# Optimization experiments

Measured on AMD Instinct MI355X. Metric: run time of the kernel, lower is better.

The kernel has to match this reference:

```python
import jax, jax.numpy as jnp
import numpy as np

B = 16384  # batch
D = 1024   # input_size (== hidden_size, required by the original code)
H = 1024   # hidden_size


def setup_inputs() -> dict:
    key = jax.random.key(0)
    ks = jax.random.split(key, 20)
    s = 0.02
    inp = {
        "x": jax.random.normal(ks[0], (B, D), dtype=jnp.float32),
        "h": jax.random.normal(ks[1], (B, H), dtype=jnp.float32),
        "c_prev": jax.random.normal(ks[2], (B, H), dtype=jnp.float32),
    }
    names = ["i_x", "f_x", "c_x", "o_x", "i_h", "f_h", "c_h", "o_h"]
    for n, name in enumerate(names):
        in_dim = D if name.endswith("_x") else H
        inp["W" + name] = jax.random.normal(ks[3 + 2 * n], (H, in_dim), dtype=jnp.float32) * s
        inp["b" + name] = jax.random.normal(ks[4 + 2 * n], (H,), dtype=jnp.float32) * s
    return inp


def reference(x, h, c_prev,
              Wi_x, bi_x, Wf_x, bf_x, Wc_x, bc_x, Wo_x, bo_x,
              Wi_h, bi_h, Wf_h, bf_h, Wc_h, bc_h, Wo_h, bo_h):
    # NOTE: the original module applies NO sigmoid to the gates; i, f, o are raw affine sums.
    i = x @ Wi_x.T + bi_x + h @ Wi_h.T + bi_h
    f = x @ Wf_x.T + bf_x + h @ Wf_h.T + bf_h
    g = jnp.tanh(x @ Wc_x.T + bc_x + h @ Wc_h.T + bc_h)
    o = x @ Wo_x.T + bo_x + h @ Wo_h.T + bo_h
    c_next = g * i + c_prev * f
    h_next = o * jnp.tanh(c_next)
    return (h_next, c_next)
```

## Files before the change

kernel.cpp:

```cpp
#include <hip/hip_runtime.h>
#include <hip/hip_bf16.h>


#define MROWS 16384
#define NCOLS 1024
#define KTOT  2048

typedef __attribute__((ext_vector_type(8))) short bf16x8;
typedef __attribute__((ext_vector_type(4))) float f32x4;
typedef unsigned int u32;
typedef unsigned short u16;

__device__ __forceinline__ u16 f2bf(float f) {
  union { float f; u32 u; } v; v.f = f;
  u32 r = v.u + 0x7fffu + ((v.u >> 16) & 1u);
  return (u16)(r >> 16);
}

__device__ __forceinline__ bf16x8 pack8(float4 lo, float4 hi) {
  bf16x8 v;
  v[0] = (short)f2bf(lo.x); v[1] = (short)f2bf(lo.y);
  v[2] = (short)f2bf(lo.z); v[3] = (short)f2bf(lo.w);
  v[4] = (short)f2bf(hi.x); v[5] = (short)f2bf(hi.y);
  v[6] = (short)f2bf(hi.z); v[7] = (short)f2bf(hi.w);
  return v;
}

__device__ __forceinline__ float tanh_fast(float x) {
  float e = __expf(2.0f * x);
  return 1.0f - 2.0f / (e + 1.0f);
}

typedef __attribute__((address_space(1))) const u32 gas_u32;
typedef __attribute__((address_space(3))) u32 las_u32;

__device__ __forceinline__ void gl_lds16(const void* g, void* l) {
  __builtin_amdgcn_global_load_lds((gas_u32*)g, (las_u32*)l, 16, 0, 0);
}

__global__ void __launch_bounds__(256) convA(const float* __restrict__ x,
                                             const float* __restrict__ h,
                                             u16* __restrict__ A) {
  u32 t = blockIdx.x * 256u + threadIdx.x;
  #pragma unroll
  for (int i = 0; i < 4; ++i) {
    u32 chunk = t + (u32)i * 1048576u;
    u32 row = chunk >> 8;
    u32 cpos = (chunk & 255u) * 8u;
    const float* src = (cpos < 1024u) ? (x + (size_t)row * 1024 + cpos)
                                      : (h + (size_t)row * 1024 + (cpos - 1024u));
    float4 lo = *(const float4*)src;
    float4 hi = *(const float4*)(src + 4);
    *(bf16x8*)(A + (size_t)chunk * 8) = pack8(lo, hi);
  }
}

__global__ void __launch_bounds__(256) convW(const float* __restrict__ wix, const float* __restrict__ wfx,
                                             const float* __restrict__ wcx, const float* __restrict__ wox,
                                             const float* __restrict__ wih, const float* __restrict__ wfh,
                                             const float* __restrict__ wch, const float* __restrict__ woh,
                                             u16* __restrict__ W) {
  u32 t = blockIdx.x * 256u + threadIdx.x;
  const float* WX[4] = {wix, wfx, wcx, wox};
  const float* WH[4] = {wih, wfh, wch, woh};
  #pragma unroll
  for (int g = 0; g < 4; ++g) {
    u32 c3 = t;
    u32 n = c3 >> 8;
    u32 cpos = (c3 & 255u) * 8u;
    const float* src = (cpos < 1024u) ? (WX[g] + (size_t)n * 1024 + cpos)
                                      : (WH[g] + (size_t)n * 1024 + (cpos - 1024u));
    float4 lo = *(const float4*)src;
    float4 hi = *(const float4*)(src + 4);
    *(bf16x8*)(W + (size_t)g * 2097152 + (size_t)c3 * 8) = pack8(lo, hi);
  }
}

__global__ void __launch_bounds__(256, 2) lstm_gemm3(
    const u16* __restrict__ Abf, const u16* __restrict__ Wbf,
    const float* __restrict__ bix, const float* __restrict__ bfx,
    const float* __restrict__ bcx, const float* __restrict__ box_,
    const float* __restrict__ bih, const float* __restrict__ bfh,
    const float* __restrict__ bch, const float* __restrict__ boh,
    const float* __restrict__ cprev, float* __restrict__ out) {
  __shared__ alignas(16) u16 sA[2 * 4096];
  __shared__ alignas(16) u16 sB[2 * 8192];

  const u32 tid = threadIdx.x;
  const u32 lane = tid & 63u;
  const u32 wid = tid >> 6;
  const u32 wr = wid >> 1, wc = wid & 1u;
  const u32 l15 = lane & 15u, l4 = lane >> 4;

  const u32 bidx = blockIdx.x;
  const u32 sid = (bidx & 7u) * 256u + (bidx >> 3);
  const u32 bm = sid >> 4, bn = sid & 15u;

  const u16* gAp[2];
  const u16* gBp[4];
  #pragma unroll
  for (int j = 0; j < 2; ++j) {
    u32 c = (wid * 2u + (u32)j) * 64u + lane;
    u32 row = c >> 2, k8 = c & 3u;
    u32 col16 = k8 ^ (row & 3u);
    gAp[j] = Abf + (size_t)(bm * 128u + row) * KTOT + col16 * 8u;
  }
  #pragma unroll
  for (int j = 0; j < 4; ++j) {
    u32 c = (wid * 4u + (u32)j) * 64u + lane;
    u32 brow = c >> 2, k8 = c & 3u;
    u32 Wrow = (brow >> 6) * 1024u + bn * 64u + (brow & 63u);
    gBp[j] = Wbf + (size_t)Wrow * KTOT + (k8 ^ (brow & 3u)) * 8u;
  }

#define STAGE(ktile, dbuf) do { \
    _Pragma("unroll") \
    for (int j = 0; j < 2; ++j) \
      gl_lds16(gAp[j] + (u32)(ktile) * 32u, sA + (dbuf) * 4096u + (wid * 2u + (u32)j) * 512u); \
    _Pragma("unroll") \
    for (int j = 0; j < 4; ++j) \
      gl_lds16(gBp[j] + (u32)(ktile) * 32u, sB + (dbuf) * 8192u + (wid * 4u + (u32)j) * 512u); \
  } while (0)

  const char* cA = (const char*)sA;
  const char* cB = (const char*)sB;

  f32x4 acc[4][4][2];
  #pragma unroll
  for (int g = 0; g < 4; ++g)
    #pragma unroll
    for (int m = 0; m < 4; ++m)
      #pragma unroll
      for (int n = 0; n < 2; ++n)
        acc[g][m][n] = (f32x4){0.f, 0.f, 0.f, 0.f};

  STAGE(0, 0);
  __syncthreads();

  #pragma unroll 2
  for (int kt = 0; kt < 64; ++kt) {
    const u32 d = (u32)kt & 1u, dn = d ^ 1u;

    if (kt < 63) STAGE(kt + 1, dn);
    __builtin_amdgcn_sched_barrier(0);

    bf16x8 af[4];
    #pragma unroll
    for (int mf = 0; mf < 4; ++mf) {
      u32 mrow = wr * 64u + (u32)mf * 16u + l15;
      af[mf] = *(const bf16x8*)(cA + d * 8192u + mrow * 64u + ((l4 ^ (mrow & 3u)) << 4));
    }

    __builtin_amdgcn_s_setprio(1);
    #pragma unroll
    for (int g = 0; g < 4; ++g)
      #pragma unroll
      for (int nf = 0; nf < 2; ++nf) {
        u32 brow = (u32)g * 64u + wc * 32u + (u32)nf * 16u + l15;
        bf16x8 bfr = *(const bf16x8*)(cB + d * 16384u + brow * 64u + ((l4 ^ (brow & 3u)) << 4));
        #pragma unroll
        for (int m = 0; m < 4; ++m)
          acc[g][m][nf] = __builtin_amdgcn_mfma_f32_16x16x32_bf16(af[m], bfr, acc[g][m][nf], 0, 0, 0);
      }
    __builtin_amdgcn_s_setprio(0);

    __syncthreads();
  }
#undef STAGE

  #pragma unroll
  for (int nf = 0; nf < 2; ++nf) {
    u32 col = bn * 64u + wc * 32u + (u32)nf * 16u + l15;
    float bi = bix[col] + bih[col];
    float bff = bfx[col] + bfh[col];
    float bc = bcx[col] + bch[col];
    float bo = box_[col] + boh[col];
    #pragma unroll
    for (int m = 0; m < 4; ++m) {
      u32 row0 = bm * 128u + wr * 64u + (u32)m * 16u + l4 * 4u;
      #pragma unroll
      for (int r = 0; r < 4; ++r) {
        size_t idx = (size_t)(row0 + (u32)r) * 1024 + col;
        float iv = acc[0][m][nf][r] + bi;
        float fv = acc[1][m][nf][r] + bff;
        float gv = tanh_fast(acc[2][m][nf][r] + bc);
        float ov = acc[3][m][nf][r] + bo;
        float cp = cprev[idx];
        float cn = gv * iv + cp * fv;
        out[idx] = ov * tanh_fast(cn);
        out[(size_t)16777216 + idx] = cn;
      }
    }
  }
}

__global__ void __launch_bounds__(256, 2) lstm_gemm_fb(
    const float* __restrict__ x, const float* __restrict__ h,
    const float* __restrict__ wix, const float* __restrict__ wfx,
    const float* __restrict__ wcx, const float* __restrict__ wox,
    const float* __restrict__ wih, const float* __restrict__ wfh,
    const float* __restrict__ wch, const float* __restrict__ woh,
    const float* __restrict__ bix, const float* __restrict__ bfx,
    const float* __restrict__ bcx, const float* __restrict__ box_,
    const float* __restrict__ bih, const float* __restrict__ bfh,
    const float* __restrict__ bch, const float* __restrict__ boh,
    const float* __restrict__ cprev, float* __restrict__ out) {
  __shared__ alignas(16) u16 sA[128 * 64];
  __shared__ alignas(16) u16 sB[4 * 64 * 64];
  const u32 tid = threadIdx.x;
  const u32 lane = tid & 63u;
  const u32 wid = tid >> 6;
  const u32 wr = wid >> 1, wc = wid & 1u;
  const u32 bidx = blockIdx.x;
  const u32 bm = bidx >> 4, bn = bidx & 15u;
  f32x4 acc[4][4][2];
  #pragma unroll
  for (int g = 0; g < 4; ++g)
    #pragma unroll
    for (int m = 0; m < 4; ++m)
      #pragma unroll
      for (int n = 0; n < 2; ++n)
        acc[g][m][n] = (f32x4){0.f, 0.f, 0.f, 0.f};
  const u32 l15 = lane & 15u, l4 = lane >> 4;
  for (int kt = 0; kt < KTOT / 64; ++kt) {
    const u32 k0 = (u32)kt * 64u;
    if (kt) __syncthreads();
    #pragma unroll
    for (int c = 0; c < 4; ++c) {
      u32 chunk = tid + (u32)c * 256u;
      u32 row = chunk >> 3;
      u32 cp = (chunk & 7u) * 8u;
      u32 gk = k0 + cp;
      const float* src = (gk < 1024u) ? (x + (size_t)(bm * 128u + row) * 1024 + gk)
                                      : (h + (size_t)(bm * 128u + row) * 1024 + (gk - 1024u));
      float4 lo = *(const float4*)src;
      float4 hi = *(const float4*)(src + 4);
      u32 dst = row * 128u + ((cp * 2u) ^ ((row & 7u) << 4));
      *(bf16x8*)((char*)sA + dst) = pack8(lo, hi);
    }
    #pragma unroll
    for (int g = 0; g < 4; ++g) {
      const float* Wxg = (g == 0) ? wix : (g == 1) ? wfx : (g == 2) ? wcx : wox;
      const float* Whg = (g == 0) ? wih : (g == 1) ? wfh : (g == 2) ? wch : woh;
      #pragma unroll
      for (int cc = 0; cc < 2; ++cc) {
        u32 c3 = tid + (u32)cc * 256u;
        u32 row = c3 >> 3;
        u32 cp = (c3 & 7u) * 8u;
        u32 gk = k0 + cp;
        const float* src = (gk < 1024u) ? (Wxg + (size_t)(bn * 64u + row) * 1024 + gk)
                                        : (Whg + (size_t)(bn * 64u + row) * 1024 + (gk - 1024u));
        float4 lo = *(const float4*)src;
        float4 hi = *(const float4*)(src + 4);
        u32 dst = (u32)g * 8192u + row * 128u + ((cp * 2u) ^ ((row & 7u) << 4));
        *(bf16x8*)((char*)sB + dst) = pack8(lo, hi);
      }
    }
    __syncthreads();
    #pragma unroll
    for (int s = 0; s < 2; ++s) {
      bf16x8 af[4];
      #pragma unroll
      for (int m = 0; m < 4; ++m) {
        u32 mrow = wr * 64u + (u32)m * 16u + l15;
        u32 off = mrow * 128u + (((u32)s * 64u + l4 * 16u) ^ ((mrow & 7u) << 4));
        af[m] = *(const bf16x8*)((const char*)sA + off);
      }
      #pragma unroll
      for (int g = 0; g < 4; ++g) {
        #pragma unroll
        for (int nf = 0; nf < 2; ++nf) {
          u32 nrow = wc * 32u + (u32)nf * 16u + l15;
          u32 off = (u32)g * 8192u + nrow * 128u +
                    (((u32)s * 64u + l4 * 16u) ^ ((nrow & 7u) << 4));
          bf16x8 bfr = *(const bf16x8*)((const char*)sB + off);
          #pragma unroll
          for (int m = 0; m < 4; ++m)
            acc[g][m][nf] = __builtin_amdgcn_mfma_f32_16x16x32_bf16(af[m], bfr, acc[g][m][nf], 0, 0, 0);
        }
      }
    }
  }
  #pragma unroll
  for (int nf = 0; nf < 2; ++nf) {
    u32 col = bn * 64u + wc * 32u + (u32)nf * 16u + l15;
    float bi = bix[col] + bih[col];
    float bff = bfx[col] + bfh[col];
    float bc = bcx[col] + bch[col];
    float bo = box_[col] + boh[col];
    #pragma unroll
    for (int m = 0; m < 4; ++m) {
      u32 row0 = bm * 128u + wr * 64u + (u32)m * 16u + l4 * 4u;
      #pragma unroll
      for (int r = 0; r < 4; ++r) {
        size_t idx = (size_t)(row0 + (u32)r) * 1024 + col;
        float iv = acc[0][m][nf][r] + bi;
        float fv = acc[1][m][nf][r] + bff;
        float gv = tanh_fast(acc[2][m][nf][r] + bc);
        float ov = acc[3][m][nf][r] + bo;
        float cp = cprev[idx];
        float cn = gv * iv + cp * fv;
        out[idx] = ov * tanh_fast(cn);
        out[(size_t)16777216 + idx] = cn;
      }
    }
  }
}

extern "C" void kernel_launch(void* const* d_in, const int* in_sizes, int n_in,
                              void* d_out, int out_size, void* d_ws, size_t ws_size,
                              hipStream_t stream) {
  const float* x = (const float*)d_in[0];
  const float* h = (const float*)d_in[1];
  const float* cprev = (const float*)d_in[2];
  const float* wix = (const float*)d_in[3];  const float* bix = (const float*)d_in[4];
  const float* wfx = (const float*)d_in[5];  const float* bfx = (const float*)d_in[6];
  const float* wcx = (const float*)d_in[7];  const float* bcx = (const float*)d_in[8];
  const float* wox = (const float*)d_in[9];  const float* box_ = (const float*)d_in[10];
  const float* wih = (const float*)d_in[11]; const float* bih = (const float*)d_in[12];
  const float* wfh = (const float*)d_in[13]; const float* bfh = (const float*)d_in[14];
  const float* wch = (const float*)d_in[15]; const float* bch = (const float*)d_in[16];
  const float* woh = (const float*)d_in[17]; const float* boh = (const float*)d_in[18];
  float* out = (float*)d_out;

  const size_t needA = (size_t)MROWS * KTOT * 2;
  const size_t needW = (size_t)4 * NCOLS * KTOT * 2;

  if (ws_size >= needA + needW) {
    u16* Abf = (u16*)d_ws;
    u16* Wbf = (u16*)((char*)d_ws + needA);
    convA<<<dim3(4096), dim3(256), 0, stream>>>(x, h, Abf);
    convW<<<dim3(1024), dim3(256), 0, stream>>>(wix, wfx, wcx, wox, wih, wfh, wch, woh, Wbf);
    lstm_gemm3<<<dim3(2048), dim3(256), 0, stream>>>(
        Abf, Wbf, bix, bfx, bcx, box_, bih, bfh, bch, boh, cprev, out);
  } else {
    lstm_gemm_fb<<<dim3(2048), dim3(256), 0, stream>>>(
        x, h, wix, wfx, wcx, wox, wih, wfh, wch, woh,
        bix, bfx, bcx, box_, bih, bfh, bch, boh, cprev, out);
  }
}
```

Measured before the change: 368.3 us.

## Fuse conversion kernels and retile GEMM to 128x32 tiles with K=64 single buffer

Merges the activation and weight bf16 conversion kernels into a single launch. Retiles the fused LSTM GEMM from 128x(4x64) tiles with double-buffered K=32 steps to 128x(4x32) tiles with a single-buffered K=64 LDS stage and an 8-way XOR swizzle, doubling the grid to 4096 blocks. This halves the accumulator registers and the number of K iterations, and drops the launch-bound occupancy hint. In exchange the load/compute overlap from double buffering is lost, with two barriers per iteration, and each block reuses less of the A tile per column.

```diff
diff --git a/kernel.cpp b/kernel.cpp
--- a/kernel.cpp
+++ b/kernel.cpp
@@ -38,158 +38,139 @@
   __builtin_amdgcn_global_load_lds((gas_u32*)g, (las_u32*)l, 16, 0, 0);
 }
 
-__global__ void __launch_bounds__(256) convA(const float* __restrict__ x,
-                                             const float* __restrict__ h,
-                                             u16* __restrict__ A) {
-  u32 t = blockIdx.x * 256u + threadIdx.x;
-  #pragma unroll
-  for (int i = 0; i < 4; ++i) {
-    u32 chunk = t + (u32)i * 1048576u;
-    u32 row = chunk >> 8;
-    u32 cpos = (chunk & 255u) * 8u;
-    const float* src = (cpos < 1024u) ? (x + (size_t)row * 1024 + cpos)
-                                      : (h + (size_t)row * 1024 + (cpos - 1024u));
-    float4 lo = *(const float4*)src;
-    float4 hi = *(const float4*)(src + 4);
-    *(bf16x8*)(A + (size_t)chunk * 8) = pack8(lo, hi);
-  }
-}
-
-__global__ void __launch_bounds__(256) convW(const float* __restrict__ wix, const float* __restrict__ wfx,
-                                             const float* __restrict__ wcx, const float* __restrict__ wox,
-                                             const float* __restrict__ wih, const float* __restrict__ wfh,
-                                             const float* __restrict__ wch, const float* __restrict__ woh,
-                                             u16* __restrict__ W) {
-  u32 t = blockIdx.x * 256u + threadIdx.x;
-  const float* WX[4] = {wix, wfx, wcx, wox};
-  const float* WH[4] = {wih, wfh, wch, woh};
-  #pragma unroll
-  for (int g = 0; g < 4; ++g) {
-    u32 c3 = t;
-    u32 n = c3 >> 8;
-    u32 cpos = (c3 & 255u) * 8u;
-    const float* src = (cpos < 1024u) ? (WX[g] + (size_t)n * 1024 + cpos)
-                                      : (WH[g] + (size_t)n * 1024 + (cpos - 1024u));
-    float4 lo = *(const float4*)src;
-    float4 hi = *(const float4*)(src + 4);
-    *(bf16x8*)(W + (size_t)g * 2097152 + (size_t)c3 * 8) = pack8(lo, hi);
-  }
-}
-
-__global__ void __launch_bounds__(256, 2) lstm_gemm3(
+__global__ void __launch_bounds__(256) convAW(
+    const float* __restrict__ x, const float* __restrict__ h,
+    const float* __restrict__ wix, const float* __restrict__ wfx,
+    const float* __restrict__ wcx, const float* __restrict__ wox,
+    const float* __restrict__ wih, const float* __restrict__ wfh,
+    const float* __restrict__ wch, const float* __restrict__ woh,
+    u16* __restrict__ A, u16* __restrict__ W) {
+  if (blockIdx.x < 4096u) {
+    u32 t = blockIdx.x * 256u + threadIdx.x;
+    #pragma unroll
+    for (int i = 0; i < 4; ++i) {
+      u32 chunk = t + (u32)i * 1048576u;
+      u32 row = chunk >> 8;
+      u32 cpos = (chunk & 255u) * 8u;
+      const float* src = (cpos < 1024u) ? (x + (size_t)row * 1024 + cpos)
+                                        : (h + (size_t)row * 1024 + (cpos - 1024u));
+      float4 lo = *(const float4*)src;
+      float4 hi = *(const float4*)(src + 4);
+      *(bf16x8*)(A + (size_t)chunk * 8) = pack8(lo, hi);
+    }
+  } else {
+    u32 t = (blockIdx.x - 4096u) * 256u + threadIdx.x;
+    const float* WX[4] = {wix, wfx, wcx, wox};
+    const float* WH[4] = {wih, wfh, wch, woh};
+    #pragma unroll
+    for (int g = 0; g < 4; ++g) {
+      u32 n = t >> 8;
+      u32 cpos = (t & 255u) * 8u;
+      const float* src = (cpos < 1024u) ? (WX[g] + (size_t)n * 1024 + cpos)
+                                        : (WH[g] + (size_t)n * 1024 + (cpos - 1024u));
+      float4 lo = *(const float4*)src;
+      float4 hi = *(const float4*)(src + 4);
+      *(bf16x8*)(W + (size_t)g * 2097152 + (size_t)t * 8) = pack8(lo, hi);
+    }
+  }
+}
+
+__global__ void __launch_bounds__(256) lstm_g128(
     const u16* __restrict__ Abf, const u16* __restrict__ Wbf,
     const float* __restrict__ bix, const float* __restrict__ bfx,
     const float* __restrict__ bcx, const float* __restrict__ box_,
     const float* __restrict__ bih, const float* __restrict__ bfh,
     const float* __restrict__ bch, const float* __restrict__ boh,
     const float* __restrict__ cprev, float* __restrict__ out) {
-  __shared__ alignas(16) u16 sA[2 * 4096];
-  __shared__ alignas(16) u16 sB[2 * 8192];
+  __shared__ alignas(16) u16 sA[8192];
+  __shared__ alignas(16) u16 sB[8192];
 
   const u32 tid = threadIdx.x;
   const u32 lane = tid & 63u;
   const u32 wid = tid >> 6;
   const u32 wr = wid >> 1, wc = wid & 1u;
   const u32 l15 = lane & 15u, l4 = lane >> 4;
+  const u32 r = lane >> 3, k8 = lane & 7u;
+  const u32 col16 = k8 ^ r;
 
   const u32 bidx = blockIdx.x;
-  const u32 sid = (bidx & 7u) * 256u + (bidx >> 3);
-  const u32 bm = sid >> 4, bn = sid & 15u;
-
-  const u16* gAp[2];
+  const u32 sid = (bidx & 7u) * 512u + (bidx >> 3);
+  const u32 bm = sid >> 5, bn = sid & 31u;
+
+  const u16* gAp[4];
   const u16* gBp[4];
   #pragma unroll
-  for (int j = 0; j < 2; ++j) {
-    u32 c = (wid * 2u + (u32)j) * 64u + lane;
-    u32 row = c >> 2, k8 = c & 3u;
-    u32 col16 = k8 ^ (row & 3u);
-    gAp[j] = Abf + (size_t)(bm * 128u + row) * KTOT + col16 * 8u;
-  }
-  #pragma unroll
   for (int j = 0; j < 4; ++j) {
-    u32 c = (wid * 4u + (u32)j) * 64u + lane;
-    u32 brow = c >> 2, k8 = c & 3u;
-    u32 Wrow = (brow >> 6) * 1024u + bn * 64u + (brow & 63u);
-    gBp[j] = Wbf + (size_t)Wrow * KTOT + (k8 ^ (brow & 3u)) * 8u;
-  }
-
-#define STAGE(ktile, dbuf) do { \
+    gAp[j] = Abf + (size_t)(bm * 128u + wid * 32u + (u32)j * 8u + r) * KTOT + col16 * 8u;
+    u32 q = wid * 4u + (u32)j;
+    u32 Wrow = ((q >> 1) & 3u) * 1024u + bn * 32u + (wid >> 1) * 16u + 8u * (q & 1u) + r;
+    gBp[j] = Wbf + (size_t)Wrow * KTOT + col16 * 8u;
+  }
+
+#define STAGE(ktile) do { \
     _Pragma("unroll") \
-    for (int j = 0; j < 2; ++j) \
-      gl_lds16(gAp[j] + (u32)(ktile) * 32u, sA + (dbuf) * 4096u + (wid * 2u + (u32)j) * 512u); \
-    _Pragma("unroll") \
-    for (int j = 0; j < 4; ++j) \
-      gl_lds16(gBp[j] + (u32)(ktile) * 32u, sB + (dbuf) * 8192u + (wid * 4u + (u32)j) * 512u); \
+    for (int j = 0; j < 4; ++j) { \
+      gl_lds16(gAp[j] + (u32)(ktile) * 64u, sA + (wid * 4u + (u32)j) * 512u); \
+      gl_lds16(gBp[j] + (u32)(ktile) * 64u, sB + (wid * 4u + (u32)j) * 512u); \
+    } \
   } while (0)
 
   const char* cA = (const char*)sA;
   const char* cB = (const char*)sB;
 
-  f32x4 acc[4][4][2];
+  f32x4 acc[4][4];
   #pragma unroll
   for (int g = 0; g < 4; ++g)
     #pragma unroll
     for (int m = 0; m < 4; ++m)
-      #pragma unroll
-      for (int n = 0; n < 2; ++n)
-        acc[g][m][n] = (f32x4){0.f, 0.f, 0.f, 0.f};
-
-  STAGE(0, 0);
-  __syncthreads();
-
-  #pragma unroll 2
-  for (int kt = 0; kt < 64; ++kt) {
-    const u32 d = (u32)kt & 1u, dn = d ^ 1u;
-
-    if (kt < 63) STAGE(kt + 1, dn);
-    __builtin_amdgcn_sched_barrier(0);
-
-    bf16x8 af[4];
-    #pragma unroll
-    for (int mf = 0; mf < 4; ++mf) {
-      u32 mrow = wr * 64u + (u32)mf * 16u + l15;
-      af[mf] = *(const bf16x8*)(cA + d * 8192u + mrow * 64u + ((l4 ^ (mrow & 3u)) << 4));
-    }
-
-    __builtin_amdgcn_s_setprio(1);
-    #pragma unroll
-    for (int g = 0; g < 4; ++g)
-      #pragma unroll
-      for (int nf = 0; nf < 2; ++nf) {
-        u32 brow = (u32)g * 64u + wc * 32u + (u32)nf * 16u + l15;
-        bf16x8 bfr = *(const bf16x8*)(cB + d * 16384u + brow * 64u + ((l4 ^ (brow & 3u)) << 4));
+      acc[g][m] = (f32x4){0.f, 0.f, 0.f, 0.f};
+
+  for (int kt = 0; kt < KTOT / 64; ++kt) {
+    if (kt) __syncthreads();
+    STAGE(kt);
+    __syncthreads();
+
+    #pragma unroll
+    for (int s = 0; s < 2; ++s) {
+      bf16x8 af[4];
+      #pragma unroll
+      for (int m = 0; m < 4; ++m) {
+        u32 mrow = wr * 64u + (u32)m * 16u + l15;
+        u32 off = mrow * 128u + (((u32)s * 64u + l4 * 16u) ^ ((mrow & 7u) << 4));
+        af[m] = *(const bf16x8*)(cA + off);
+      }
+      #pragma unroll
+      for (int g = 0; g < 4; ++g) {
+        u32 frow = wc * 64u + (u32)g * 16u + l15;
+        u32 off = frow * 128u + (((u32)s * 64u + l4 * 16u) ^ ((frow & 7u) << 4));
+        bf16x8 bfr = *(const bf16x8*)(cB + off);
         #pragma unroll
         for (int m = 0; m < 4; ++m)
-          acc[g][m][nf] = __builtin_amdgcn_mfma_f32_16x16x32_bf16(af[m], bfr, acc[g][m][nf], 0, 0, 0);
-      }
-    __builtin_amdgcn_s_setprio(0);
-
-    __syncthreads();
+          acc[g][m] = __builtin_amdgcn_mfma_f32_16x16x32_bf16(af[m], bfr, acc[g][m], 0, 0, 0);
+      }
+    }
   }
 #undef STAGE
 
-  #pragma unroll
-  for (int nf = 0; nf < 2; ++nf) {
-    u32 col = bn * 64u + wc * 32u + (u32)nf * 16u + l15;
-    float bi = bix[col] + bih[col];
-    float bff = bfx[col] + bfh[col];
-    float bc = bcx[col] + bch[col];
-    float bo = box_[col] + boh[col];
-    #pragma unroll
-    for (int m = 0; m < 4; ++m) {
-      u32 row0 = bm * 128u + wr * 64u + (u32)m * 16u + l4 * 4u;
-      #pragma unroll
-      for (int r = 0; r < 4; ++r) {
-        size_t idx = (size_t)(row0 + (u32)r) * 1024 + col;
-        float iv = acc[0][m][nf][r] + bi;
-        float fv = acc[1][m][nf][r] + bff;
-        float gv = tanh_fast(acc[2][m][nf][r] + bc);
-        float ov = acc[3][m][nf][r] + bo;
-        float cp = cprev[idx];
-        float cn = gv * iv + cp * fv;
-        out[idx] = ov * tanh_fast(cn);
-        out[(size_t)16777216 + idx] = cn;
-      }
+  const u32 col = bn * 32u + wc * 16u + l15;
+  const float bi = bix[col] + bih[col];
+  const float bff = bfx[col] + bfh[col];
+  const float bc = bcx[col] + bch[col];
+  const float bo = box_[col] + boh[col];
+  #pragma unroll
+  for (int m = 0; m < 4; ++m) {
+    u32 row0 = bm * 128u + wr * 64u + (u32)m * 16u + l4 * 4u;
+    #pragma unroll
+    for (int rr = 0; rr < 4; ++rr) {
+      size_t idx = (size_t)(row0 + (u32)rr) * 1024 + col;
+      float iv = acc[0][m][rr] + bi;
+      float fv = acc[1][m][rr] + bff;
+      float gv = tanh_fast(acc[2][m][rr] + bc);
+      float ov = acc[3][m][rr] + bo;
+      float cp = cprev[idx];
+      float cn = gv * iv + cp * fv;
+      out[idx] = ov * tanh_fast(cn);
+      out[(size_t)16777216 + idx] = cn;
     }
   }
 }
@@ -292,12 +273,12 @@
     for (int m = 0; m < 4; ++m) {
       u32 row0 = bm * 128u + wr * 64u + (u32)m * 16u + l4 * 4u;
       #pragma unroll
-      for (int r = 0; r < 4; ++r) {
-        size_t idx = (size_t)(row0 + (u32)r) * 1024 + col;
-        float iv = acc[0][m][nf][r] + bi;
-        float fv = acc[1][m][nf][r] + bff;
-        float gv = tanh_fast(acc[2][m][nf][r] + bc);
-        float ov = acc[3][m][nf][r] + bo;
+      for (int rr = 0; rr < 4; ++rr) {
+        size_t idx = (size_t)(row0 + (u32)rr) * 1024 + col;
+        float iv = acc[0][m][nf][rr] + bi;
+        float fv = acc[1][m][nf][rr] + bff;
+        float gv = tanh_fast(acc[2][m][nf][rr] + bc);
+        float ov = acc[3][m][nf][rr] + bo;
         float cp = cprev[idx];
         float cn = gv * iv + cp * fv;
         out[idx] = ov * tanh_fast(cn);
@@ -329,9 +310,9 @@
   if (ws_size >= needA + needW) {
     u16* Abf = (u16*)d_ws;
     u16* Wbf = (u16*)((char*)d_ws + needA);
-    convA<<<dim3(4096), dim3(256), 0, stream>>>(x, h, Abf);
-    convW<<<dim3(1024), dim3(256), 0, stream>>>(wix, wfx, wcx, wox, wih, wfh, wch, woh, Wbf);
-    lstm_gemm3<<<dim3(2048), dim3(256), 0, stream>>>(
+    convAW<<<dim3(5120), dim3(256), 0, stream>>>(
+        x, h, wix, wfx, wcx, wox, wih, wfh, wch, woh, Abf, Wbf);
+    lstm_g128<<<dim3(4096), dim3(256), 0, stream>>>(
         Abf, Wbf, bix, bfx, bcx, box_, bih, bfh, bch, boh, cprev, out);
   } else {
     lstm_gemm_fb<<<dim3(2048), dim3(256), 0, stream>>>(
```

After: 375.7 us. 2.0% more time.
